# Kernel tuning notes

Hardware: AMD Instinct MI355X
Metric: run time of the kernel (lower is better)

## Reference

```python
import jax, jax.numpy as jnp
import numpy as np

NUM_NODES = 80000
V_GLOBALS = 50000
N = 32      # grapharea_size
D = 300     # feature dim
R = 4       # num relations
E = 64      # edges per timestep
B, T = 2, 64


def setup_inputs() -> dict:
    key = jax.random.key(0)
    ks = jax.random.split(key, 10)
    return {
        "x_indices": jax.random.randint(ks[0], (B, T, N), 0, NUM_NODES, dtype=jnp.int32),
        "edge_index": jax.random.randint(ks[1], (B, T, 2, E), 0, N, dtype=jnp.int32),
        "edge_type": jax.random.randint(ks[2], (B, T, E), 0, R, dtype=jnp.int32),
        "X": jax.random.normal(ks[3], (NUM_NODES, D), jnp.float32) * 0.1,
        "conv_W": jax.random.normal(ks[4], (R, D, D), jnp.float32) * (1.0 / np.sqrt(D)),
        "W_0": jax.random.normal(ks[5], (D, D), jnp.float32) * (1.0 / np.sqrt(D)),
        "update_gate_W": jax.random.normal(ks[6], (N * D, D), jnp.float32) * (1.0 / np.sqrt(N * D)),
        "update_gate_U": jax.random.normal(ks[7], (D, D), jnp.float32) * (1.0 / np.sqrt(D)),
        "lin_w": jax.random.normal(ks[8], (V_GLOBALS, D), jnp.float32) * (1.0 / np.sqrt(D)),
        "lin_b": jax.random.normal(ks[9], (V_GLOBALS,), jnp.float32) * 0.01,
    }


def _rgcn_step(X, conv_W, W_0, Wg, Ug, lin_w, lin_b, mem, idx, ei, et):
    # gather grapharea features: [N, D]
    gx = X[idx]
    src, dst = ei[0], ei[1]
    n = gx.shape[0]
    r = conv_W.shape[0]
    # per-relation linear transform: [R, N, D]
    xw = jnp.einsum('nd,rde->rne', gx, conv_W)
    # edge-type masks emulate split_edge_index: [R, E]
    mask = (et[None, :] == jnp.arange(r, dtype=et.dtype)[:, None]).astype(gx.dtype)
    # GCN symmetric normalization with self-loops (deg includes self-loop weight 1)
    deg = jax.vmap(lambda w: jax.ops.segment_sum(w, dst, num_segments=n))(mask) + 1.0  # [R, N]
    dis = jax.lax.rsqrt(deg)
    norm = dis[:, src] * dis[:, dst] * mask                      # [R, E]
    msgs = xw[:, src, :] * norm[..., None]                       # [R, E, D]
    agg = jax.vmap(lambda m: jax.ops.segment_sum(m, dst, num_segments=n))(msgs)
    agg = agg + xw * (dis ** 2)[..., None]                       # self-loop messages
    composite = agg.sum(0)                                       # sum over relations, [N, D]
    # eye(N) @ (gx @ W_0) == gx @ W_0
    proposed = composite + gx @ W_0
    # GRU-style update gate from flattened grapharea + previous memory's first node
    u = jax.nn.sigmoid(gx.reshape(-1) @ Wg + mem[0] @ Ug)        # [D]
    new = u[None, :] * proposed + (1.0 - u[None, :]) * mem       # [N, D]
    x1 = jax.nn.leaky_relu(new)[0]                               # current node, [D]
    logits = x1 @ lin_w.T + lin_b                                # [V]
    return new, jax.nn.log_softmax(logits)


def reference(x_indices, edge_index, edge_type, X, conv_W, W_0, update_gate_W, update_gate_U, lin_w, lin_b):
    b, t, n = x_indices.shape
    s = b * t
    idxs = x_indices.reshape(s, n)
    eis = edge_index.reshape(s, 2, -1)
    ets = edge_type.reshape(s, -1)

    def step(mem, inp):
        idx, ei, et = inp
        new, logp = _rgcn_step(X, conv_W, W_0, update_gate_W, update_gate_U,
                               lin_w, lin_b, mem, idx, ei, et)
        # memory carry is a non-grad buffer updated via .data.copy_ in torch
        return jax.lax.stop_gradient(new), logp

    mem0 = jnp.zeros((n, X.shape[1]), X.dtype)
    _, preds_globals = jax.lax.scan(step, mem0, (idxs, eis, ets))  # [S, V]
    preds_senses = jnp.zeros((s,), X.dtype)  # include_senses=False -> stacked zeros
    return preds_globals, preds_senses
```

## Files before the change

### kernel.cpp

```cpp
#include <hip/hip_runtime.h>

#define S 128
#define N 32
#define D 300
#define DP 320
#define E 64
#define R 4
#define V 50000
#define VP 50048
#define ND 9600
#define KY 1504
#define DPAD 304

typedef unsigned short ushortT;
typedef __attribute__((ext_vector_type(8))) short short8;
typedef __attribute__((ext_vector_type(4))) short short4v;
typedef __attribute__((ext_vector_type(4))) float floatx4;
typedef __attribute__((ext_vector_type(2))) _Float16 half2v;
typedef __attribute__((ext_vector_type(19))) unsigned int uintx19;

#if defined(__has_builtin)
#if __has_builtin(__builtin_amdgcn_fdot2)
#define HAVE_FDOT2 1
#endif
#endif

__device__ inline float bf2f(ushortT h) {
    unsigned u = ((unsigned)h) << 16;
    float f;
    __builtin_memcpy(&f, &u, 4);
    return f;
}

__device__ inline float bfbits_lo(unsigned u) {
    unsigned b = u << 16;
    float f;
    __builtin_memcpy(&f, &b, 4);
    return f;
}

__device__ inline float bfbits_hi(unsigned u) {
    unsigned b = u & 0xffff0000u;
    float f;
    __builtin_memcpy(&f, &b, 4);
    return f;
}

__device__ inline ushortT f2bf(float f) {
    unsigned u;
    __builtin_memcpy(&u, &f, 4);
    unsigned r = (u + 0x7fffu + ((u >> 16) & 1u)) >> 16;
    return (ushortT)r;
}

__device__ inline float ldf(const void* p, size_t i, int isb) {
    return isb ? bf2f(((const ushortT*)p)[i]) : ((const float*)p)[i];
}

__device__ inline float dot2f(unsigned a, unsigned b, float c) {
    half2v av, bv;
    __builtin_memcpy(&av, &a, 4);
    __builtin_memcpy(&bv, &b, 4);
#if defined(HAVE_FDOT2)
    return __builtin_amdgcn_fdot2(av, bv, c, false);
#else
    return fmaf((float)av[1], (float)bv[1], fmaf((float)av[0], (float)bv[0], c));
#endif
}

__device__ inline unsigned packh2(float lo, float hi) {
    half2v h;
    h[0] = (_Float16)lo;
    h[1] = (_Float16)hi;
    unsigned u;
    __builtin_memcpy(&u, &h, 4);
    return u;
}

__global__ void k_detect(const void* X, int* flag) {
    __shared__ int bad;
    if (threadIdx.x == 0) bad = 0;
    __syncthreads();
    const ushortT* p = (const ushortT*)X;
    int b = 0;
    for (int i = threadIdx.x; i < 4096; i += 256) {
        float v = bf2f(p[i]);
        if (!(v > -2.f && v < 2.f)) b = 1;
    }
    if (b) atomicOr(&bad, 1);
    __syncthreads();
    if (threadIdx.x == 0) flag[0] = bad ? 0 : 1;
}

__global__ void k_gatherb(const int* __restrict__ flag, const int* __restrict__ xi,
                          const void* __restrict__ X, ushortT* __restrict__ gxb) {
    int isb = flag[0];
    int sn = blockIdx.x;
    int d = threadIdx.x;
    if (d < D) {
        int node = xi[sn];
        ushortT v = isb ? ((const ushortT*)X)[(size_t)node * D + d]
                        : f2bf(((const float*)X)[(size_t)node * D + d]);
        gxb[(size_t)sn * D + d] = v;
    }
}

__global__ void k_twg(const int* __restrict__ flag, const void* __restrict__ Wg,
                      ushortT* __restrict__ wgt) {
    int isb = flag[0];
    __shared__ float tile[32][33];
    int k0 = blockIdx.x * 32, d0 = blockIdx.y * 32;
    int tx = threadIdx.x & 31, ty = threadIdx.x >> 5;
    for (int i = ty; i < 32; i += 8) {
        int d = d0 + tx;
        tile[i][tx] = (d < D) ? ldf(Wg, (size_t)(k0 + i) * D + d, isb) : 0.f;
    }
    __syncthreads();
    for (int i = ty; i < 32; i += 8) {
        int d = d0 + i;
        if (d < DPAD) wgt[(size_t)d * ND + k0 + tx] = f2bf(tile[tx][i]);
    }
}

__global__ void k_tws(const int* __restrict__ flag, const void* __restrict__ convW,
                      const void* __restrict__ W0, ushortT* __restrict__ wst) {
    int isb = flag[0];
    __shared__ float tile[32][33];
    int k0 = blockIdx.x * 32, d0 = blockIdx.y * 32;
    int tx = threadIdx.x & 31, ty = threadIdx.x >> 5;
    for (int i = ty; i < 32; i += 8) {
        int kp = k0 + i, d = d0 + tx;
        float v = 0.f;
        if (d < D && kp < 1500)
            v = (kp < 1200) ? ldf(convW, (size_t)kp * D + d, isb)
                            : ldf(W0, (size_t)(kp - 1200) * D + d, isb);
        tile[i][tx] = v;
    }
    __syncthreads();
    for (int i = ty; i < 32; i += 8) {
        int d = d0 + i;
        if (d < DPAD) wst[(size_t)d * KY + k0 + tx] = f2bf(tile[tx][i]);
    }
}

__global__ void k_yb(const ushortT* __restrict__ gxb, const int* __restrict__ ei,
                     const int* __restrict__ et, ushortT* __restrict__ yb) {
    int s = blockIdx.x;
    int t = threadIdx.x;
    __shared__ int se[E], de[E], te[E];
    __shared__ float disv[R][N];
    if (t < E) {
        se[t] = ei[(size_t)s * 2 * E + t];
        de[t] = ei[(size_t)s * 2 * E + E + t];
        te[t] = et[(size_t)s * E + t];
    }
    __syncthreads();
    if (t < R * N) {
        int r = t >> 5, n = t & 31;
        float c = 1.f;
        for (int e = 0; e < E; ++e) c += (te[e] == r && de[e] == n) ? 1.f : 0.f;
        disv[r][n] = rsqrtf(c);
    }
    __syncthreads();
    if (t < D) {
        const ushortT* g = gxb + (size_t)s * ND;
        float g0 = bf2f(g[t]);
        float yy[R];
#pragma unroll
        for (int r = 0; r < R; ++r) yy[r] = g0 * disv[r][0] * disv[r][0];
        for (int e = 0; e < E; ++e) {
            if (de[e] == 0) {
                int r = te[e];
                yy[r] += disv[r][se[e]] * disv[r][0] * bf2f(g[(size_t)se[e] * D + t]);
            }
        }
#pragma unroll
        for (int r = 0; r < R; ++r) yb[(size_t)s * KY + r * D + t] = f2bf(yy[r]);
        yb[(size_t)s * KY + 4 * D + t] = g[t];
    }
    if (t < 4) yb[(size_t)s * KY + 1500 + t] = 0;
}

__global__ __launch_bounds__(256) void k_gemm(const ushortT* __restrict__ A, int lda,
                                              const ushortT* __restrict__ Bt, int ldb,
                                              float* __restrict__ C, int ldc, int ncols,
                                              int kchunks, int per) {
    int wave = threadIdx.x >> 6, lane = threadIdx.x & 63;
    int col = lane & 15, quad = lane >> 4;
    int m0 = blockIdx.x * 16, n0 = blockIdx.y * 16;
    int z = blockIdx.z;
    int kbeg = z * per;
    int kend = kbeg + per;
    if (kend > kchunks) kend = kchunks;
    floatx4 acc = {0.f, 0.f, 0.f, 0.f};
    const ushortT* ap = A + (size_t)(m0 + col) * lda + quad * 8;
    const ushortT* bp = Bt + (size_t)(n0 + col) * ldb + quad * 8;
    for (int kc = kbeg + wave; kc < kend; kc += 4) {
        short8 a = *(const short8*)(ap + kc * 32);
        short8 b = *(const short8*)(bp + kc * 32);
        acc = __builtin_amdgcn_mfma_f32_16x16x32_bf16(a, b, acc, 0, 0, 0);
    }
    __shared__ float red[4][64][4];
#pragma unroll
    for (int i = 0; i < 4; ++i) red[wave][lane][i] = acc[i];
    __syncthreads();
    if (wave == 0) {
#pragma unroll
        for (int i = 0; i < 4; ++i) {
            float v = red[0][lane][i] + red[1][lane][i] + red[2][lane][i] + red[3][lane][i];
            int m = m0 + quad * 4 + i;
            int n = n0 + col;
            if (n < ncols) C[(size_t)z * S * ldc + (size_t)m * ldc + n] = v;
        }
    }
}

__global__ void k_red(const float* __restrict__ part, float* __restrict__ out, int n, int nz) {
    int i = blockIdx.x * 256 + threadIdx.x;
    if (i < n) {
        float v = 0.f;
        for (int z = 0; z < nz; ++z) v += part[(size_t)z * n + i];
        out[i] = v;
    }
}

__global__ __attribute__((amdgpu_flat_work_group_size(512, 512), amdgpu_waves_per_eu(2, 2))) void
k_scan(const int* __restrict__ flag, const float* __restrict__ a, const float* __restrict__ P0,
       const void* __restrict__ Ug, ushortT* __restrict__ x1p) {
    int isb = flag[0];
    int t = threadIdx.x;
    int w = t >> 6, lane = t & 63;
    int kbase = w * 38;
    int myk = kbase + lane;
    bool red_ok = (lane < 38) && (myk < D);
    int d4 = 256 + lane;
    bool d4ok = d4 < D;
    uintx19 UV0, UV1, UV2, UV3, UV4;
#pragma unroll
    for (int j = 0; j < 19; ++j) {
        int k1 = kbase + 2 * j, k2 = k1 + 1;
        bool k1ok = k1 < D, k2ok = k2 < D;
        UV0[j] = packh2(k1ok ? ldf(Ug, (size_t)k1 * D + lane, isb) : 0.f,
                        k2ok ? ldf(Ug, (size_t)k2 * D + lane, isb) : 0.f);
        UV1[j] = packh2(k1ok ? ldf(Ug, (size_t)k1 * D + 64 + lane, isb) : 0.f,
                        k2ok ? ldf(Ug, (size_t)k2 * D + 64 + lane, isb) : 0.f);
        UV2[j] = packh2(k1ok ? ldf(Ug, (size_t)k1 * D + 128 + lane, isb) : 0.f,
                        k2ok ? ldf(Ug, (size_t)k2 * D + 128 + lane, isb) : 0.f);
        UV3[j] = packh2(k1ok ? ldf(Ug, (size_t)k1 * D + 192 + lane, isb) : 0.f,
                        k2ok ? ldf(Ug, (size_t)k2 * D + 192 + lane, isb) : 0.f);
        UV4[j] = packh2((k1ok && d4ok) ? ldf(Ug, (size_t)k1 * D + d4, isb) : 0.f,
                        (k2ok && d4ok) ? ldf(Ug, (size_t)k2 * D + d4, isb) : 0.f);
    }
    for (int i = t; i < S * 20; i += 512) {
        int s = i / 20, d = 300 + (i % 20);
        x1p[(size_t)s * DP + d] = 0;
    }
    __shared__ float part[8][320];
    __shared__ unsigned msh16[2][160];
    for (int i = t; i < 320; i += 512) ((unsigned*)msh16)[i] = 0;
    float mreg = 0.f;
    int buf = 0;
    __syncthreads();
    for (int s = 0; s < S; ++s) {
        float av = 0.f, pv = 0.f;
        if (red_ok) {
            av = a[s * D + myk];
            pv = P0[s * D + myk];
        }
        uintx19 MV;
#pragma unroll
        for (int j = 0; j < 19; ++j) MV[j] = msh16[buf][w * 20 + j];
        float acc0 = 0.f, acc1 = 0.f, acc2 = 0.f, acc3 = 0.f, acc4 = 0.f;
#pragma unroll
        for (int j = 0; j < 19; ++j) {
            unsigned md = MV[j];
            acc0 = dot2f(UV0[j], md, acc0);
            acc1 = dot2f(UV1[j], md, acc1);
            acc2 = dot2f(UV2[j], md, acc2);
            acc3 = dot2f(UV3[j], md, acc3);
            acc4 = dot2f(UV4[j], md, acc4);
        }
        part[w][lane] = acc0;
        part[w][64 + lane] = acc1;
        part[w][128 + lane] = acc2;
        part[w][192 + lane] = acc3;
        part[w][256 + lane] = acc4;
        __syncthreads();
        if (red_ok) {
            float pr = av;
#pragma unroll
            for (int w2 = 0; w2 < 8; ++w2) pr += part[w2][myk];
            float u = 1.f / (1.f + __expf(-pr));
            float nm = u * pv + (1.f - u) * mreg;
            mreg = nm;
            _Float16 mh = (_Float16)nm;
            ushortT mb;
            __builtin_memcpy(&mb, &mh, 2);
            ((ushortT*)&msh16[buf ^ 1][0])[w * 40 + lane] = mb;
            float x = nm > 0.f ? nm : 0.01f * nm;
            x1p[(size_t)s * DP + myk] = f2bf(x);
        }
        __syncthreads();
        buf ^= 1;
    }
}

__global__ __launch_bounds__(256) void k_logits(const int* __restrict__ flag,
                                                const ushortT* __restrict__ x1p,
                                                const void* __restrict__ lw,
                                                const void* __restrict__ lb,
                                                void* __restrict__ out) {
    int isb = flag[0];
    int wave = threadIdx.x >> 6, lane = threadIdx.x & 63;
    int col = lane & 15, quad = lane >> 4;
    int v = blockIdx.x * 64 + wave * 16 + col;
    int vv = v < V ? v : V - 1;
    floatx4 acc[8];
#pragma unroll
    for (int i = 0; i < 8; ++i) acc[i] = (floatx4){0.f, 0.f, 0.f, 0.f};
#pragma unroll
    for (int kc = 0; kc < 9; ++kc) {
        int k0 = kc * 32 + quad * 8;
        short8 b;
        if (isb) {
            const ushortT* bp = (const ushortT*)lw + (size_t)vv * D + k0;
            short4v lo = *(const short4v*)bp;
            short4v hi = *(const short4v*)(bp + 4);
            b = (short8){lo[0], lo[1], lo[2], lo[3], hi[0], hi[1], hi[2], hi[3]};
        } else {
            const float* bp = (const float*)lw + (size_t)vv * D + k0;
            floatx4 f0 = *(const floatx4*)bp;
            floatx4 f1 = *(const floatx4*)(bp + 4);
            b = (short8){(short)f2bf(f0[0]), (short)f2bf(f0[1]), (short)f2bf(f0[2]),
                         (short)f2bf(f0[3]), (short)f2bf(f1[0]), (short)f2bf(f1[1]),
                         (short)f2bf(f1[2]), (short)f2bf(f1[3])};
        }
#pragma unroll
        for (int st = 0; st < 8; ++st) {
            short8 aa = *(const short8*)(x1p + (size_t)(st * 16 + col) * DP + k0);
            acc[st] = __builtin_amdgcn_mfma_f32_16x16x32_bf16(aa, b, acc[st], 0, 0, 0);
        }
    }
    {
        int k0 = 288 + quad * 8;
        short8 b;
#pragma unroll
        for (int j = 0; j < 8; ++j) {
            int k = k0 + j;
            ushortT bv = 0;
            if (k < D)
                bv = isb ? ((const ushortT*)lw)[(size_t)vv * D + k]
                         : f2bf(((const float*)lw)[(size_t)vv * D + k]);
            b[j] = (short)bv;
        }
#pragma unroll
        for (int st = 0; st < 8; ++st) {
            short8 aa = *(const short8*)(x1p + (size_t)(st * 16 + col) * DP + k0);
            acc[st] = __builtin_amdgcn_mfma_f32_16x16x32_bf16(aa, b, acc[st], 0, 0, 0);
        }
    }
    if (v < V) {
        float bias = ldf(lb, v, isb);
#pragma unroll
        for (int st = 0; st < 8; ++st) {
#pragma unroll
            for (int i = 0; i < 4; ++i) {
                int s = st * 16 + quad * 4 + i;
                float val = acc[st][i] + bias;
                if (isb)
                    ((ushortT*)out)[(size_t)s * V + v] = f2bf(val);
                else
                    ((float*)out)[(size_t)s * V + v] = val;
            }
        }
    }
}

__global__ __launch_bounds__(512) void k_norm(const int* __restrict__ flag,
                                              void* __restrict__ out) {
    int isb = flag[0];
    int s = blockIdx.x;
    int t = threadIdx.x;
    __shared__ float red[512];
    if (s == 0 && t < S) {
        if (isb)
            ((ushortT*)out)[(size_t)S * V + t] = 0;
        else
            ((float*)out)[(size_t)S * V + t] = 0.f;
    }
    float mx = -1e30f;
    if (isb) {
        const uint4* row = (const uint4*)((const ushortT*)out + (size_t)s * V);
        for (int i = t; i < 6250; i += 512) {
            uint4 q = row[i];
            mx = fmaxf(mx, fmaxf(fmaxf(bfbits_lo(q.x), bfbits_hi(q.x)),
                                 fmaxf(bfbits_lo(q.y), bfbits_hi(q.y))));
            mx = fmaxf(mx, fmaxf(fmaxf(bfbits_lo(q.z), bfbits_hi(q.z)),
                                 fmaxf(bfbits_lo(q.w), bfbits_hi(q.w))));
        }
    } else {
        const floatx4* row = (const floatx4*)((const float*)out + (size_t)s * V);
        for (int i = t; i < 12500; i += 512) {
            floatx4 q = row[i];
            mx = fmaxf(mx, fmaxf(fmaxf(q[0], q[1]), fmaxf(q[2], q[3])));
        }
    }
    red[t] = mx;
    __syncthreads();
    for (int o = 256; o > 0; o >>= 1) {
        if (t < o) red[t] = fmaxf(red[t], red[t + o]);
        __syncthreads();
    }
    float M = red[0];
    __syncthreads();
    float sm = 0.f;
    if (isb) {
        const uint4* row = (const uint4*)((const ushortT*)out + (size_t)s * V);
        for (int i = t; i < 6250; i += 512) {
            uint4 q = row[i];
            sm += __expf(bfbits_lo(q.x) - M) + __expf(bfbits_hi(q.x) - M) +
                  __expf(bfbits_lo(q.y) - M) + __expf(bfbits_hi(q.y) - M) +
                  __expf(bfbits_lo(q.z) - M) + __expf(bfbits_hi(q.z) - M) +
                  __expf(bfbits_lo(q.w) - M) + __expf(bfbits_hi(q.w) - M);
        }
    } else {
        const floatx4* row = (const floatx4*)((const float*)out + (size_t)s * V);
        for (int i = t; i < 12500; i += 512) {
            floatx4 q = row[i];
            sm += __expf(q[0] - M) + __expf(q[1] - M) + __expf(q[2] - M) + __expf(q[3] - M);
        }
    }
    red[t] = sm;
    __syncthreads();
    for (int o = 256; o > 0; o >>= 1) {
        if (t < o) red[t] += red[t + o];
        __syncthreads();
    }
    float lse = M + __logf(red[0]);
    if (isb) {
        uint4* row = (uint4*)((ushortT*)out + (size_t)s * V);
        for (int i = t; i < 6250; i += 512) {
            uint4 q = row[i];
            uint4 o;
            o.x = (unsigned)f2bf(bfbits_lo(q.x) - lse) |
                  ((unsigned)f2bf(bfbits_hi(q.x) - lse) << 16);
            o.y = (unsigned)f2bf(bfbits_lo(q.y) - lse) |
                  ((unsigned)f2bf(bfbits_hi(q.y) - lse) << 16);
            o.z = (unsigned)f2bf(bfbits_lo(q.z) - lse) |
                  ((unsigned)f2bf(bfbits_hi(q.z) - lse) << 16);
            o.w = (unsigned)f2bf(bfbits_lo(q.w) - lse) |
                  ((unsigned)f2bf(bfbits_hi(q.w) - lse) << 16);
            row[i] = o;
        }
    } else {
        floatx4* row = (floatx4*)((float*)out + (size_t)s * V);
        for (int i = t; i < 12500; i += 512) {
            floatx4 q = row[i];
            q[0] -= lse;
            q[1] -= lse;
            q[2] -= lse;
            q[3] -= lse;
            row[i] = q;
        }
    }
}

#define OFF_FLAG 0
#define OFF_GXB 256
#define OFF_WGT 2457856
#define OFF_WST 8294656
#define OFF_YB 9209088
#define OFF_A 9594112
#define OFF_P0 9747712
#define OFF_X1P 9901312
#define OFF_STATS 9983232
#define OFF_PART 9983744
#define PART_A_BYTES (4 * S * D * 4)
#define PART_P_BYTES (2 * S * D * 4)

extern "C" void kernel_launch(void* const* d_in, const int* in_sizes, int n_in, void* d_out,
                              int out_size, void* d_ws, size_t ws_size, hipStream_t stream) {
    const int* xi = (const int*)d_in[0];
    const int* ei = (const int*)d_in[1];
    const int* et = (const int*)d_in[2];
    const void* X = d_in[3];
    const void* convW = d_in[4];
    const void* W0 = d_in[5];
    const void* Wg = d_in[6];
    const void* Ug = d_in[7];
    const void* lw = d_in[8];
    const void* lb = d_in[9];
    char* ws = (char*)d_ws;

    int* flag = (int*)(ws + OFF_FLAG);
    ushortT* gxb = (ushortT*)(ws + OFF_GXB);
    ushortT* wgt = (ushortT*)(ws + OFF_WGT);
    ushortT* wst = (ushortT*)(ws + OFF_WST);
    ushortT* yb = (ushortT*)(ws + OFF_YB);
    float* a = (float*)(ws + OFF_A);
    float* P0 = (float*)(ws + OFF_P0);
    ushortT* x1p = (ushortT*)(ws + OFF_X1P);

    bool split = ws_size >= (size_t)(OFF_PART + PART_A_BYTES + PART_P_BYTES);
    int nza = split ? 4 : 1;
    int nzp = split ? 2 : 1;
    float* apart = split ? (float*)(ws + OFF_PART) : a;
    float* ppart = split ? (float*)(ws + OFF_PART + PART_A_BYTES) : P0;
    int pera = (ND / 32 + nza - 1) / nza;
    int perp = (KY / 32 + nzp - 1) / nzp;

    hipLaunchKernelGGL(k_detect, dim3(1), dim3(256), 0, stream, X, flag);
    hipLaunchKernelGGL(k_gatherb, dim3(S * N), dim3(DP), 0, stream, flag, xi, X, gxb);
    hipLaunchKernelGGL(k_twg, dim3(ND / 32, 10), dim3(256), 0, stream, flag, Wg, wgt);
    hipLaunchKernelGGL(k_tws, dim3(KY / 32, 10), dim3(256), 0, stream, flag, convW, W0, wst);
    hipLaunchKernelGGL(k_yb, dim3(S), dim3(DP), 0, stream, gxb, ei, et, yb);
    hipLaunchKernelGGL(k_gemm, dim3(S / 16, 19, nza), dim3(256), 0, stream, gxb, ND, wgt, ND,
                       apart, D, D, ND / 32, pera);
    if (split)
        hipLaunchKernelGGL(k_red, dim3((S * D + 255) / 256), dim3(256), 0, stream, apart, a,
                           S * D, nza);
    hipLaunchKernelGGL(k_gemm, dim3(S / 16, 19, nzp), dim3(256), 0, stream, yb, KY, wst, KY,
                       ppart, D, D, KY / 32, perp);
    if (split)
        hipLaunchKernelGGL(k_red, dim3((S * D + 255) / 256), dim3(256), 0, stream, ppart, P0,
                           S * D, nzp);
    hipLaunchKernelGGL(k_scan, dim3(1), dim3(512), 0, stream, flag, a, P0, Ug, x1p);
    hipLaunchKernelGGL(k_logits, dim3(VP / 64), dim3(256), 0, stream, flag, x1p, lw, lb, d_out);
    hipLaunchKernelGGL(k_norm, dim3(S), dim3(512), 0, stream, flag, d_out);
}
```

Baseline: 411.8 us.

## Widen GRU scan to 16 waves and drop the second barrier per step

The serial gate scan now runs with 1024 threads, so each wave handles 20 hidden dimensions instead of 38. That roughly halves the per-step dot-product chain and the register-held Ug slice. The partial-sum buffer is double-buffered, and each wave only reads the memory entries it wrote itself. Together these remove the trailing __syncthreads in each of the 128 steps. In exchange, the reduction now sums 16 partials instead of 8, and the kernel runs more waves on a single workgroup.

```diff
diff --git a/kernel.cpp b/kernel.cpp
--- a/kernel.cpp
+++ b/kernel.cpp
@@ -17,7 +17,7 @@
 typedef __attribute__((ext_vector_type(4))) short short4v;
 typedef __attribute__((ext_vector_type(4))) float floatx4;
 typedef __attribute__((ext_vector_type(2))) _Float16 half2v;
-typedef __attribute__((ext_vector_type(19))) unsigned int uintx19;
+typedef __attribute__((ext_vector_type(10))) unsigned int uintx10;
 
 #if defined(__has_builtin)
 #if __has_builtin(__builtin_amdgcn_fdot2)
@@ -224,20 +224,20 @@
     }
 }
 
-__global__ __attribute__((amdgpu_flat_work_group_size(512, 512), amdgpu_waves_per_eu(2, 2))) void
+__global__ __launch_bounds__(1024) void
 k_scan(const int* __restrict__ flag, const float* __restrict__ a, const float* __restrict__ P0,
        const void* __restrict__ Ug, ushortT* __restrict__ x1p) {
     int isb = flag[0];
     int t = threadIdx.x;
     int w = t >> 6, lane = t & 63;
-    int kbase = w * 38;
+    int kbase = w * 20;
     int myk = kbase + lane;
-    bool red_ok = (lane < 38) && (myk < D);
+    bool red_ok = (lane < 20) && (myk < D);
     int d4 = 256 + lane;
     bool d4ok = d4 < D;
-    uintx19 UV0, UV1, UV2, UV3, UV4;
-#pragma unroll
-    for (int j = 0; j < 19; ++j) {
+    uintx10 UV0, UV1, UV2, UV3, UV4;
+#pragma unroll
+    for (int j = 0; j < 10; ++j) {
         int k1 = kbase + 2 * j, k2 = k1 + 1;
         bool k1ok = k1 < D, k2ok = k2 < D;
         UV0[j] = packh2(k1ok ? ldf(Ug, (size_t)k1 * D + lane, isb) : 0.f,
@@ -251,13 +251,13 @@
         UV4[j] = packh2((k1ok && d4ok) ? ldf(Ug, (size_t)k1 * D + d4, isb) : 0.f,
                         (k2ok && d4ok) ? ldf(Ug, (size_t)k2 * D + d4, isb) : 0.f);
     }
-    for (int i = t; i < S * 20; i += 512) {
+    for (int i = t; i < S * 20; i += 1024) {
         int s = i / 20, d = 300 + (i % 20);
         x1p[(size_t)s * DP + d] = 0;
     }
-    __shared__ float part[8][320];
-    __shared__ unsigned msh16[2][160];
-    for (int i = t; i < 320; i += 512) ((unsigned*)msh16)[i] = 0;
+    __shared__ float part[2][16][320];
+    __shared__ unsigned msh16[160];
+    for (int i = t; i < 160; i += 1024) msh16[i] = 0;
     float mreg = 0.f;
     int buf = 0;
     __syncthreads();
@@ -267,12 +267,12 @@
             av = a[s * D + myk];
             pv = P0[s * D + myk];
         }
-        uintx19 MV;
-#pragma unroll
-        for (int j = 0; j < 19; ++j) MV[j] = msh16[buf][w * 20 + j];
+        uintx10 MV;
+#pragma unroll
+        for (int j = 0; j < 10; ++j) MV[j] = msh16[w * 10 + j];
         float acc0 = 0.f, acc1 = 0.f, acc2 = 0.f, acc3 = 0.f, acc4 = 0.f;
 #pragma unroll
-        for (int j = 0; j < 19; ++j) {
+        for (int j = 0; j < 10; ++j) {
             unsigned md = MV[j];
             acc0 = dot2f(UV0[j], md, acc0);
             acc1 = dot2f(UV1[j], md, acc1);
@@ -280,27 +280,33 @@
             acc3 = dot2f(UV3[j], md, acc3);
             acc4 = dot2f(UV4[j], md, acc4);
         }
-        part[w][lane] = acc0;
-        part[w][64 + lane] = acc1;
-        part[w][128 + lane] = acc2;
-        part[w][192 + lane] = acc3;
-        part[w][256 + lane] = acc4;
+        part[buf][w][lane] = acc0;
+        part[buf][w][64 + lane] = acc1;
+        part[buf][w][128 + lane] = acc2;
+        part[buf][w][192 + lane] = acc3;
+        part[buf][w][256 + lane] = acc4;
         __syncthreads();
         if (red_ok) {
-            float pr = av;
-#pragma unroll
-            for (int w2 = 0; w2 < 8; ++w2) pr += part[w2][myk];
+            float q0 = part[buf][0][myk] + part[buf][1][myk];
+            float q1 = part[buf][2][myk] + part[buf][3][myk];
+            float q2 = part[buf][4][myk] + part[buf][5][myk];
+            float q3 = part[buf][6][myk] + part[buf][7][myk];
+            float q4 = part[buf][8][myk] + part[buf][9][myk];
+            float q5 = part[buf][10][myk] + part[buf][11][myk];
+            float q6 = part[buf][12][myk] + part[buf][13][myk];
+            float q7 = part[buf][14][myk] + part[buf][15][myk];
+            float r0 = q0 + q1, r1 = q2 + q3, r2 = q4 + q5, r3 = q6 + q7;
+            float pr = av + ((r0 + r1) + (r2 + r3));
             float u = 1.f / (1.f + __expf(-pr));
             float nm = u * pv + (1.f - u) * mreg;
             mreg = nm;
             _Float16 mh = (_Float16)nm;
             ushortT mb;
             __builtin_memcpy(&mb, &mh, 2);
-            ((ushortT*)&msh16[buf ^ 1][0])[w * 40 + lane] = mb;
+            ((ushortT*)msh16)[myk] = mb;
             float x = nm > 0.f ? nm : 0.01f * nm;
             x1p[(size_t)s * DP + myk] = f2bf(x);
         }
-        __syncthreads();
         buf ^= 1;
     }
 }
@@ -524,7 +530,7 @@
     if (split)
         hipLaunchKernelGGL(k_red, dim3((S * D + 255) / 256), dim3(256), 0, stream, ppart, P0,
                            S * D, nzp);
-    hipLaunchKernelGGL(k_scan, dim3(1), dim3(512), 0, stream, flag, a, P0, Ug, x1p);
+    hipLaunchKernelGGL(k_scan, dim3(1), dim3(1024), 0, stream, flag, a, P0, Ug, x1p);
     hipLaunchKernelGGL(k_logits, dim3(VP / 64), dim3(256), 0, stream, flag, x1p, lw, lb, d_out);
     hipLaunchKernelGGL(k_norm, dim3(S), dim3(512), 0, stream, flag, d_out);
 }
```

After: 445.2 us. 8.1% more time.
